# Kernel optimization log

Measured on AMD Instinct MI355X. Metric: run time of the kernel, lower is better.

Reference implementation:

```python
import jax, jax.numpy as jnp
import numpy as np

B, S, E, L = 8, 2048, 512, 128


def setup_inputs() -> dict:
    key = jax.random.key(0)
    k1, k2 = jax.random.split(key)
    embeddings = jax.random.normal(k1, (B, S, E), dtype=jnp.float32)
    means = jax.random.normal(k2, (L, E), dtype=jnp.float32)
    var = jnp.ones((E,), dtype=jnp.float32)  # default init: requires_grad=False, ones
    return {"embeddings": embeddings, "means": means, "var": var}


def reference(embeddings, means, var):
    # Diagonal-Gaussian log-density per (token, label):
    #   log_density - 0.5 * sum_e (means[l,e] - emb[b,s,e])^2 / var[e]
    # Rewritten as GEMM + per-row/per-label norms (avoids [B,S,L,E] intermediate).
    n_embed = embeddings.shape[-1]
    factor = -n_embed / 2.0 * (np.log(2.0) + np.log(np.pi))
    # After init_params: log_density = factor - 0.5 * sum(log var); var=ones -> factor.
    log_density = factor - 0.5 * jnp.sum(jnp.log(var))
    inv_var = 1.0 / var  # [E]
    e2 = jnp.einsum('bse,e->bs', embeddings * embeddings, inv_var)      # [B,S]
    m2 = jnp.einsum('le,e->l', means * means, inv_var)                  # [L]
    cross = jnp.einsum('bse,le->bsl', embeddings, means * inv_var)      # [B,S,L]
    sq_mahalanobis = e2[..., None] + m2[None, None, :] - 2.0 * cross    # [B,S,L]
    return log_density - 0.5 * sq_mahalanobis
```

## Files before the change

### kernel.cpp

```cpp
#include <hip/hip_runtime.h>
#include <math.h>

#define EDIM 512
#define LDIM 128
#define MTOT 16384
#define TM 16
#define BK 64
#define NCHUNK (EDIM / BK)
#define LSTR 72

typedef __attribute__((ext_vector_type(8))) short s8v;
typedef __attribute__((ext_vector_type(4))) short s4v;
typedef __attribute__((ext_vector_type(4))) float f4v;

__device__ __forceinline__ unsigned short f2bf(float x) {
    union { float f; unsigned u; } c; c.f = x;
    return (unsigned short)((c.u + 0x7fffu + ((c.u >> 16) & 1u)) >> 16);
}

__device__ __forceinline__ void ld_lds16(const void* g, void* l) {
    __builtin_amdgcn_global_load_lds(
        (const __attribute__((address_space(1))) unsigned int*)g,
        (__attribute__((address_space(3))) unsigned int*)l, 16, 0, 0);
}

__global__ __launch_bounds__(64) void gs_prep(
    const float* __restrict__ means, const float* __restrict__ var,
    unsigned short* __restrict__ Bfrag, float* __restrict__ m2,
    float* __restrict__ ivbuf, float* __restrict__ coef)
{
    const int l = blockIdx.x;
    const int t = threadIdx.x;
    const int e0 = t * 8;

    float mv[8], iv[8];
    const float* mrow = means + l * EDIM + e0;
#pragma unroll
    for (int i = 0; i < 8; ++i) { mv[i] = mrow[i]; iv[i] = 1.0f / var[e0 + i]; }

    float part = 0.0f;
    s8v pr;
#pragma unroll
    for (int i = 0; i < 8; ++i) {
        float p = mv[i] * iv[i];
        pr[i] = (short)f2bf(p);
        part += mv[i] * p;
    }
    {
        const int kc   = t >> 3;
        const int ks_i = (t >> 2) & 1;
        const int q    = t & 3;
        const int F    = ks_i * 8 + (l >> 4);
        const int ln   = q * 16 + (l & 15);
        *(s8v*)(Bfrag + kc * 8192 + F * 512 + ln * 8) = pr;
    }

#pragma unroll
    for (int off = 32; off > 0; off >>= 1) part += __shfl_down(part, off, 64);
    if (t == 0) m2[l] = part;

    if (l == 0) {
#pragma unroll
        for (int i = 0; i < 8; ++i) ivbuf[e0 + i] = iv[i];
        float ld = 0.0f;
#pragma unroll
        for (int i = 0; i < 8; ++i) ld += logf(var[e0 + i]);
#pragma unroll
        for (int off = 32; off > 0; off >>= 1) ld += __shfl_down(ld, off, 64);
        if (t == 0) {
            const float factor = -(float)EDIM * 0.5f * 1.8378770664093453f;
            *coef = factor - 0.5f * ld;
        }
    }
}

__global__ __launch_bounds__(256, 4) void gs_main(
    const float* __restrict__ emb, const unsigned short* __restrict__ Bfrag,
    const float* __restrict__ m2, const float* __restrict__ ivbuf,
    const float* __restrict__ coef, float* __restrict__ out)
{
    __shared__ __align__(16) unsigned short Alds[2][TM][LSTR];
    __shared__ __align__(16) unsigned short Blds[2][16 * 64 * 8];
    __shared__ float e2part[256];
    __shared__ float e2s[TM];

    const int t    = threadIdx.x;
    const int lane = t & 63;
    const int w    = t >> 6;
    const int q    = lane >> 4;
    const int fr   = lane & 15;
    const int m0   = blockIdx.x * TM;

    const int arow = t >> 4;
    const int kseg = (t & 15) * 4;

    const float* ap  = emb   + (size_t)(m0 + arow) * EDIM + kseg;
    const float* ivp = ivbuf + kseg;

    f4v acc[2];
    acc[0] = (f4v)0.0f; acc[1] = (f4v)0.0f;
    float e2acc = 0.0f;

    f4v ar[2], vr[2];
    ar[0] = *(const f4v*)(ap);        ar[1] = *(const f4v*)(ap + BK);
    vr[0] = *(const f4v*)(ivp);       vr[1] = *(const f4v*)(ivp + BK);

#define STAGE_B(kc, buf)                                                       \
    {                                                                          \
        const char* sb = (const char*)Bfrag + (kc) * 16384 + w * 4096;         \
        char*       db = (char*)&Blds[buf][0] + w * 4096;                      \
        _Pragma("unroll")                                                      \
        for (int j = 0; j < 4; ++j)                                            \
            ld_lds16(sb + j * 1024 + lane * 16, db + j * 1024);                \
    }

    STAGE_B(0, 0)

#pragma unroll
    for (int kc = 0; kc < NCHUNK; ++kc) {
        const int b = kc & 1;

        f4v xa = ar[b], va = vr[b];
        s4v a4;
#pragma unroll
        for (int i = 0; i < 4; ++i) {
            a4[i] = (short)f2bf(xa[i]);
            e2acc += xa[i] * xa[i] * va[i];
        }
        *(s4v*)&Alds[b][arow][kseg] = a4;

        __syncthreads();

        if (kc + 1 < NCHUNK) STAGE_B(kc + 1, b ^ 1)
        if (kc + 2 < NCHUNK) {
            ar[b] = *(const f4v*)(ap + (kc + 2) * BK);
            vr[b] = *(const f4v*)(ivp + (kc + 2) * BK);
        }

#pragma unroll
        for (int ks_i = 0; ks_i < 2; ++ks_i) {
            s8v af = *(const s8v*)&Alds[b][fr][ks_i * 32 + q * 8];
#pragma unroll
            for (int ct = 0; ct < 2; ++ct) {
                const int F = ks_i * 8 + w * 2 + ct;
                s8v bfv = *(const s8v*)&Blds[b][F * 512 + lane * 8];
                acc[ct] = __builtin_amdgcn_mfma_f32_16x16x32_bf16(af, bfv, acc[ct], 0, 0, 0);
            }
        }
    }

    e2part[t] = e2acc;
    __syncthreads();
    if (t < TM) {
        float s = 0.0f;
#pragma unroll
        for (int j = 0; j < 16; ++j) s += e2part[t * 16 + j];
        e2s[t] = s;
    }
    __syncthreads();

    const float cf = *coef;
#pragma unroll
    for (int ct = 0; ct < 2; ++ct) {
        const int n = (w * 2 + ct) * 16 + fr;
        const float cm = cf - 0.5f * m2[n];
#pragma unroll
        for (int r = 0; r < 4; ++r) {
            const int row = q * 4 + r;
            out[(size_t)(m0 + row) * LDIM + n] = acc[ct][r] + cm - 0.5f * e2s[row];
        }
    }
#undef STAGE_B
}

extern "C" void kernel_launch(void* const* d_in, const int* in_sizes, int n_in,
                              void* d_out, int out_size, void* d_ws, size_t ws_size,
                              hipStream_t stream) {
    const float* emb   = (const float*)d_in[0];
    const float* means = (const float*)d_in[1];
    const float* var   = (const float*)d_in[2];
    float* out = (float*)d_out;

    char* ws = (char*)d_ws;
    unsigned short* Bfrag = (unsigned short*)ws;
    float* m2    = (float*)(ws + 131072);
    float* ivbuf = (float*)(ws + 131584);
    float* coef  = (float*)(ws + 133632);

    gs_prep<<<LDIM, 64, 0, stream>>>(means, var, Bfrag, m2, ivbuf, coef);
    gs_main<<<MTOT / TM, 256, 0, stream>>>(emb, Bfrag, m2, ivbuf, coef, out);
}
```

Baseline: 86.03 us.

## Make waves independent: redundant A staging per wave, B fragments in registers

Each wave now loads and converts the full 16-row A tile into its own private LDS slice, and loads its B fragments straight from global memory into registers instead of staging them through shared LDS. This removes all block-wide __syncthreads from the K loop and the e2 reduction, which now uses intra-wave shuffles. In exchange, each block reads the embedding tile four times (once per wave) and does the bf16 conversion redundantly, which raises global/L2 traffic and VALU work.

```diff
diff --git a/kernel.cpp b/kernel.cpp
--- a/kernel.cpp
+++ b/kernel.cpp
@@ -6,8 +6,8 @@
 #define MTOT 16384
 #define TM 16
 #define BK 64
-#define NCHUNK (EDIM / BK)
-#define LSTR 72
+#define NCHUNK 8
+#define LSTR 76
 
 typedef __attribute__((ext_vector_type(8))) short s8v;
 typedef __attribute__((ext_vector_type(4))) short s4v;
@@ -16,12 +16,6 @@
 __device__ __forceinline__ unsigned short f2bf(float x) {
     union { float f; unsigned u; } c; c.f = x;
     return (unsigned short)((c.u + 0x7fffu + ((c.u >> 16) & 1u)) >> 16);
-}
-
-__device__ __forceinline__ void ld_lds16(const void* g, void* l) {
-    __builtin_amdgcn_global_load_lds(
-        (const __attribute__((address_space(1))) unsigned int*)g,
-        (__attribute__((address_space(3))) unsigned int*)l, 16, 0, 0);
 }
 
 __global__ __launch_bounds__(64) void gs_prep(
@@ -79,10 +73,7 @@
     const float* __restrict__ m2, const float* __restrict__ ivbuf,
     const float* __restrict__ coef, float* __restrict__ out)
 {
-    __shared__ __align__(16) unsigned short Alds[2][TM][LSTR];
-    __shared__ __align__(16) unsigned short Blds[2][16 * 64 * 8];
-    __shared__ float e2part[256];
-    __shared__ float e2s[TM];
+    __shared__ __align__(16) unsigned short Alds[4][2][TM][LSTR];
 
     const int t    = threadIdx.x;
     const int lane = t & 63;
@@ -91,86 +82,97 @@
     const int fr   = lane & 15;
     const int m0   = blockIdx.x * TM;
 
-    const int arow = t >> 4;
-    const int kseg = (t & 15) * 4;
+    const float* ap  = emb + ((size_t)m0 + q * 4) * EDIM + fr * 4;
+    const float* ivp = ivbuf + fr * 4;
 
-    const float* ap  = emb   + (size_t)(m0 + arow) * EDIM + kseg;
-    const float* ivp = ivbuf + kseg;
+#define LOAD_A(kc, slot)                                                   \
+    {                                                                      \
+        _Pragma("unroll")                                                  \
+        for (int s = 0; s < 4; ++s)                                        \
+            ax[slot][s] = *(const f4v*)(ap + s * EDIM + (kc) * BK);        \
+        vx[slot] = *(const f4v*)(ivp + (kc) * BK);                         \
+    }
+
+#define LOAD_B(kc, slot)                                                   \
+    {                                                                      \
+        _Pragma("unroll")                                                  \
+        for (int ks = 0; ks < 2; ++ks)                                     \
+            _Pragma("unroll")                                              \
+            for (int j = 0; j < 2; ++j)                                    \
+                bx[slot][ks][j] = *(const s8v*)(Bfrag + (kc) * 8192        \
+                                   + (ks * 8 + w * 2 + j) * 512 + lane * 8); \
+    }
+
+#define CVT_A(slot)                                                        \
+    {                                                                      \
+        _Pragma("unroll")                                                  \
+        for (int s = 0; s < 4; ++s) {                                      \
+            s4v a4;                                                        \
+            _Pragma("unroll")                                              \
+            for (int i = 0; i < 4; ++i) {                                  \
+                const float x = ax[slot][s][i];                            \
+                a4[i] = (short)f2bf(x);                                    \
+                e2p[s] += x * x * vx[slot][i];                             \
+            }                                                              \
+            *(s4v*)&Alds[w][slot][q * 4 + s][fr * 4] = a4;                 \
+        }                                                                  \
+    }
 
     f4v acc[2];
     acc[0] = (f4v)0.0f; acc[1] = (f4v)0.0f;
-    float e2acc = 0.0f;
+    float e2p[4] = {0.0f, 0.0f, 0.0f, 0.0f};
 
-    f4v ar[2], vr[2];
-    ar[0] = *(const f4v*)(ap);        ar[1] = *(const f4v*)(ap + BK);
-    vr[0] = *(const f4v*)(ivp);       vr[1] = *(const f4v*)(ivp + BK);
+    f4v ax[2][4];
+    f4v vx[2];
+    s8v bx[2][2][2];
 
-#define STAGE_B(kc, buf)                                                       \
-    {                                                                          \
-        const char* sb = (const char*)Bfrag + (kc) * 16384 + w * 4096;         \
-        char*       db = (char*)&Blds[buf][0] + w * 4096;                      \
-        _Pragma("unroll")                                                      \
-        for (int j = 0; j < 4; ++j)                                            \
-            ld_lds16(sb + j * 1024 + lane * 16, db + j * 1024);                \
-    }
-
-    STAGE_B(0, 0)
+    LOAD_A(0, 0)
+    LOAD_B(0, 0)
+    LOAD_A(1, 1)
+    LOAD_B(1, 1)
+    CVT_A(0)
 
 #pragma unroll
     for (int kc = 0; kc < NCHUNK; ++kc) {
         const int b = kc & 1;
 
-        f4v xa = ar[b], va = vr[b];
-        s4v a4;
+        if (kc + 2 < NCHUNK) LOAD_A(kc + 2, b)
+
+        if (kc + 1 < NCHUNK) CVT_A(!b)
+
 #pragma unroll
-        for (int i = 0; i < 4; ++i) {
-            a4[i] = (short)f2bf(xa[i]);
-            e2acc += xa[i] * xa[i] * va[i];
-        }
-        *(s4v*)&Alds[b][arow][kseg] = a4;
-
-        __syncthreads();
-
-        if (kc + 1 < NCHUNK) STAGE_B(kc + 1, b ^ 1)
-        if (kc + 2 < NCHUNK) {
-            ar[b] = *(const f4v*)(ap + (kc + 2) * BK);
-            vr[b] = *(const f4v*)(ivp + (kc + 2) * BK);
+        for (int ks = 0; ks < 2; ++ks) {
+            s8v af = *(const s8v*)&Alds[w][b][fr][ks * 32 + q * 8];
+#pragma unroll
+            for (int j = 0; j < 2; ++j)
+                acc[j] = __builtin_amdgcn_mfma_f32_16x16x32_bf16(af, bx[b][ks][j], acc[j], 0, 0, 0);
         }
 
-#pragma unroll
-        for (int ks_i = 0; ks_i < 2; ++ks_i) {
-            s8v af = *(const s8v*)&Alds[b][fr][ks_i * 32 + q * 8];
-#pragma unroll
-            for (int ct = 0; ct < 2; ++ct) {
-                const int F = ks_i * 8 + w * 2 + ct;
-                s8v bfv = *(const s8v*)&Blds[b][F * 512 + lane * 8];
-                acc[ct] = __builtin_amdgcn_mfma_f32_16x16x32_bf16(af, bfv, acc[ct], 0, 0, 0);
-            }
-        }
+        if (kc + 2 < NCHUNK) LOAD_B(kc + 2, b)
     }
 
-    e2part[t] = e2acc;
-    __syncthreads();
-    if (t < TM) {
-        float s = 0.0f;
 #pragma unroll
-        for (int j = 0; j < 16; ++j) s += e2part[t * 16 + j];
-        e2s[t] = s;
+    for (int s = 0; s < 4; ++s) {
+        e2p[s] += __shfl_xor(e2p[s], 1, 64);
+        e2p[s] += __shfl_xor(e2p[s], 2, 64);
+        e2p[s] += __shfl_xor(e2p[s], 4, 64);
+        e2p[s] += __shfl_xor(e2p[s], 8, 64);
     }
-    __syncthreads();
 
     const float cf = *coef;
 #pragma unroll
-    for (int ct = 0; ct < 2; ++ct) {
-        const int n = (w * 2 + ct) * 16 + fr;
+    for (int j = 0; j < 2; ++j) {
+        const int n = (w * 2 + j) * 16 + fr;
         const float cm = cf - 0.5f * m2[n];
 #pragma unroll
         for (int r = 0; r < 4; ++r) {
             const int row = q * 4 + r;
-            out[(size_t)(m0 + row) * LDIM + n] = acc[ct][r] + cm - 0.5f * e2s[row];
+            out[(size_t)(m0 + row) * LDIM + n] = acc[j][r] + cm - 0.5f * e2p[r];
         }
     }
-#undef STAGE_B
+#undef LOAD_A
+#undef LOAD_B
+#undef CVT_A
 }
 
 extern "C" void kernel_launch(void* const* d_in, const int* in_sizes, int n_in,
```

Measured after the change: 111.5 us. +29.6%, slower.
